# Kernel optimization log

Hardware: AMD Instinct MI355X
Metric: run time of the kernel (lower is better)

## Reference

```python
import jax, jax.numpy as jnp
import numpy as np

N_NODES = 100000
NEG_SLOPE = 0.2

def _glorot(key, shape):
    lim = float(np.sqrt(6.0 / (shape[0] + shape[-1])))
    return jax.random.uniform(key, shape, jnp.float32, -lim, lim)

def setup_inputs() -> dict:
    key = jax.random.key(0)
    ks = jax.random.split(key, 12)
    x = jax.random.normal(ks[0], (N_NODES, 128), jnp.float32)
    edge_index = jax.random.randint(ks[1], (2, 3200000), 0, N_NODES).astype(jnp.int64)
    # layer 1: in=128, heads=2, out=8
    W1 = _glorot(ks[2], (128, 16)); a_src1 = _glorot(ks[3], (2, 8)); a_dst1 = _glorot(ks[4], (2, 8)); b1 = jnp.zeros((16,), jnp.float32)
    # layer 2: in=16, heads=2, out=4
    W2 = _glorot(ks[5], (16, 8)); a_src2 = _glorot(ks[6], (2, 4)); a_dst2 = _glorot(ks[7], (2, 4)); b2 = jnp.zeros((8,), jnp.float32)
    # layer 3: in=8, heads=1, out=4
    W3 = _glorot(ks[8], (8, 4)); a_src3 = _glorot(ks[9], (1, 4)); a_dst3 = _glorot(ks[10], (1, 4)); b3 = jnp.zeros((4,), jnp.float32)
    Wc = _glorot(ks[11], (4, 2)); bc = jnp.zeros((2,), jnp.float32)
    return {"x": x, "edge_index": edge_index,
            "W1": W1, "a_src1": a_src1, "a_dst1": a_dst1, "b1": b1,
            "W2": W2, "a_src2": a_src2, "a_dst2": a_dst2, "b2": b2,
            "W3": W3, "a_src3": a_src3, "a_dst3": a_dst3, "b3": b3,
            "Wc": Wc, "bc": bc}

def gat_layer(x, src, dst, W, a_src, a_dst, b, H, C):
    # PyG GATConv: linear -> per-node attention terms -> per-edge leaky_relu -> segment softmax over dst -> scatter-sum
    N = x.shape[0]
    h = (x @ W).reshape(N, H, C)                         # [N,H,C]
    alpha_s = jnp.sum(h * a_src, axis=-1)                # [N,H]
    alpha_d = jnp.sum(h * a_dst, axis=-1)                # [N,H]
    e = jax.nn.leaky_relu(alpha_s[src] + alpha_d[dst], NEG_SLOPE)  # [E,H]
    m = jax.ops.segment_max(e, dst, num_segments=N)      # [N,H]
    ex = jnp.exp(e - m[dst])
    denom = jax.ops.segment_sum(ex, dst, num_segments=N)
    alpha = ex / (denom[dst] + 1e-16)                    # [E,H]
    out = jax.ops.segment_sum(h[src] * alpha[:, :, None], dst, num_segments=N)  # [N,H,C]
    return out.reshape(N, H * C) + b

def reference(x, edge_index, W1, a_src1, a_dst1, b1, W2, a_src2, a_dst2, b2, W3, a_src3, a_dst3, b3, Wc, bc):
    N = x.shape[0]
    loop = jnp.arange(N, dtype=edge_index.dtype)
    src = jnp.concatenate([edge_index[0], loop])  # add_self_loops=True (PyG default)
    dst = jnp.concatenate([edge_index[1], loop])
    h = jax.nn.relu(gat_layer(x, src, dst, W1, a_src1, a_dst1, b1, 2, 8))
    h = jax.nn.relu(gat_layer(h, src, dst, W2, a_src2, a_dst2, b2, 2, 4))
    # dropout p=0.5 is identity in eval mode
    h = gat_layer(h, src, dst, W3, a_src3, a_dst3, b3, 1, 4)
    return h @ Wc + bc
```

## Files before the change

### kernel.cpp

```cpp
#include <hip/hip_runtime.h>

#define TB 256
#define NGRP 8
#define NB_P 512
#define TBP 256
#define NBKT 256
#define SORT_T 1024
#define STG_CAP 14336
#define STG2_CAP 6400

typedef int      i4v __attribute__((ext_vector_type(4)));
typedef float    f4v __attribute__((ext_vector_type(4)));
typedef _Float16 h4v __attribute__((ext_vector_type(4)));
typedef _Float16 h8v __attribute__((ext_vector_type(8)));

struct __align__(16) Rec2 { _Float16 h[8]; float as[2]; float pad[2]; };
struct __align__(16) Rec3 { _Float16 h[4]; float as; float pad; };

static __device__ __forceinline__ float leaky(float x) {
  return x > 0.f ? x : 0.2f * x;
}


__global__ void k_bcount(const int* __restrict__ dstA, int* __restrict__ cnt,
                         int E4, int E, unsigned M, int CH4) {
  __shared__ int lc[4 * NBKT];
  for (int i = threadIdx.x; i < 4 * NBKT; i += TBP) lc[i] = 0;
  __syncthreads();
  int* lcw = lc + (threadIdx.x >> 6) * NBKT;
  const int bstart = blockIdx.x * CH4;
  const int bend = min(E4, bstart + CH4);
  const i4v* d4 = reinterpret_cast<const i4v*>(dstA);
  for (int i = bstart + threadIdx.x; i < bend; i += TBP) {
    i4v d = __builtin_nontemporal_load(&d4[i]);
#pragma unroll
    for (int k = 0; k < 4; ++k) atomicAdd(&lcw[__umulhi((unsigned)d[k], M)], 1);
  }
  if (blockIdx.x == NB_P - 1) {
    for (int t = E4 * 4 + threadIdx.x; t < E; t += TBP)
      atomicAdd(&lcw[__umulhi((unsigned)dstA[t], M)], 1);
  }
  __syncthreads();
  for (int b = threadIdx.x; b < NBKT; b += TBP)
    cnt[b * NB_P + blockIdx.x] = lc[b] + lc[NBKT + b] + lc[2 * NBKT + b] + lc[3 * NBKT + b];
}

__global__ void k_bscan1(const int* __restrict__ cnt, int* __restrict__ off,
                         int* __restrict__ colTotal) {
  __shared__ int sh[NB_P];
  const int t = threadIdx.x;
  const int b = blockIdx.x;
  int v = cnt[b * NB_P + t];
  sh[t] = v;
  __syncthreads();
  for (int o = 1; o < NB_P; o <<= 1) {
    int u = (t >= o) ? sh[t - o] : 0;
    __syncthreads();
    sh[t] += u;
    __syncthreads();
  }
  off[b * NB_P + t] = sh[t] - v;
  if (t == NB_P - 1) colTotal[b] = sh[t];
}

__global__ void k_bscan2(const int* __restrict__ colTotal, int* __restrict__ bucketBase) {
  __shared__ int sh[NBKT];
  const int t = threadIdx.x;
  int v = colTotal[t];
  sh[t] = v;
  __syncthreads();
  for (int o = 1; o < NBKT; o <<= 1) {
    int u = (t >= o) ? sh[t - o] : 0;
    __syncthreads();
    sh[t] += u;
    __syncthreads();
  }
  bucketBase[t] = sh[t] - v;
  if (t == NBKT - 1) bucketBase[NBKT] = sh[t];
}

__global__ void k_bscatter(const int* __restrict__ srcA, const int* __restrict__ dstA,
                           const int* __restrict__ cnt, const int* __restrict__ off,
                           const int* __restrict__ bucketBase, int* __restrict__ epk,
                           int E4, int E, unsigned M, int R, int CH4) {
  __shared__ int loff[NBKT + 1];
  __shared__ int lcur[NBKT];
  __shared__ int gbase[NBKT];
  __shared__ int stg[STG2_CAP];
  const int t = threadIdx.x;
  {
    int v = cnt[t * NB_P + blockIdx.x];
    loff[t] = v;
    __syncthreads();
    for (int o = 1; o < NBKT; o <<= 1) {
      int u = (t >= o) ? loff[t - o] : 0;
      __syncthreads();
      loff[t] += u;
      __syncthreads();
    }
    int incl = loff[t];
    __syncthreads();
    loff[t] = incl - v;
    lcur[t] = incl - v;
    if (t == NBKT - 1) loff[NBKT] = incl;
    gbase[t] = bucketBase[t] + off[t * NB_P + blockIdx.x];
  }
  __syncthreads();
  const int bstart = blockIdx.x * CH4;
  const int bend = min(E4, bstart + CH4);
  const i4v* d4 = reinterpret_cast<const i4v*>(dstA);
  const i4v* s4 = reinterpret_cast<const i4v*>(srcA);
  for (int i = bstart + t; i < bend; i += TBP) {
    i4v d = __builtin_nontemporal_load(&d4[i]);
    i4v sv = __builtin_nontemporal_load(&s4[i]);
#pragma unroll
    for (int k = 0; k < 4; ++k) {
      int dd = d[k];
      int b = __umulhi((unsigned)dd, M);
      int pos = atomicAdd(&lcur[b], 1);
      stg[pos] = ((dd - b * R) << 17) | sv[k];
    }
  }
  if (blockIdx.x == NB_P - 1) {
    for (int i = E4 * 4 + t; i < E; i += TBP) {
      int dd = dstA[i];
      int b = __umulhi((unsigned)dd, M);
      int pos = atomicAdd(&lcur[b], 1);
      stg[pos] = ((dd - b * R) << 17) | srcA[i];
    }
  }
  __syncthreads();
  const int total = loff[NBKT];
  for (int i = t; i < total; i += TBP) {
    int loQ = 0, hiQ = NBKT;
#pragma unroll
    for (int it = 0; it < 8; ++it) {
      int mid = (loQ + hiQ) >> 1;
      if (loff[mid] <= i) loQ = mid; else hiQ = mid;
    }
    epk[gbase[loQ] + (i - loff[loQ])] = stg[i];
  }
}

__global__ void k_bsort(const int* __restrict__ epk, const int* __restrict__ bucketBase,
                        int* __restrict__ rowStart, int* __restrict__ colIdx,
                        int N, int R, int E) {
  __shared__ int sc[512];
  __shared__ int stg[STG_CAP];
  const int b = (blockIdx.x & (NGRP - 1)) * (NBKT / NGRP) + (blockIdx.x >> 3);
  const int lo = bucketBase[b], hi = bucketBase[b + 1];
  const int cnt = hi - lo;
  const int nodeLo = b * R;
  const int nN = min(R, N - nodeLo);
  const int t = threadIdx.x;
  if (t < 512) sc[t] = 0;
  __syncthreads();
  for (int i = lo + t; i < hi; i += SORT_T) {
    int pk = __builtin_nontemporal_load(&epk[i]);
    atomicAdd(&sc[pk >> 17], 1);
  }
  __syncthreads();
  int own = (t < 512) ? sc[t] : 0;
  for (int o = 1; o < 512; o <<= 1) {
    int u = (t < 512 && t >= o) ? sc[t - o] : 0;
    __syncthreads();
    if (t < 512) sc[t] += u;
    __syncthreads();
  }
  if (t < nN) rowStart[nodeLo + t] = lo + sc[t] - own;
  if (b == NBKT - 1 && t == 0) rowStart[N] = E;
  if (t < 512) sc[t] -= own;
  __syncthreads();
  if (cnt <= STG_CAP) {
    for (int i = lo + t; i < hi; i += SORT_T) {
      int pk = epk[i];
      int pos = atomicAdd(&sc[pk >> 17], 1);
      stg[pos] = pk & 0x1FFFF;
    }
    __syncthreads();
    for (int i = t; i < cnt; i += SORT_T) colIdx[lo + i] = stg[i];
  } else {
    for (int i = lo + t; i < hi; i += SORT_T) {
      int pk = epk[i];
      int pos = lo + atomicAdd(&sc[pk >> 17], 1);
      colIdx[pos] = pk & 0x1FFFF;
    }
  }
}


template <int IN, int H, int C, int SPLIT, bool NT>
__global__ void k_node(const float* __restrict__ xin, const float* __restrict__ W,
                       const float* __restrict__ a_src, const float* __restrict__ a_dst,
                       _Float16* __restrict__ hout, float* __restrict__ as_,
                       float* __restrict__ ad_, int N) {
  constexpr int OUT = H * C;
  constexpr int PIN4 = IN / SPLIT / 4;
  constexpr int NPB = TB / SPLIT;
  __shared__ float Ws[IN * OUT];
  __shared__ float As[OUT], Ad[OUT];
  for (int i = threadIdx.x; i < IN * OUT; i += blockDim.x) Ws[i] = W[i];
  if (threadIdx.x < OUT) {
    As[threadIdx.x] = a_src[threadIdx.x];
    Ad[threadIdx.x] = a_dst[threadIdx.x];
  }
  __syncthreads();
  const int j = threadIdx.x & (SPLIT - 1);
  const int n = blockIdx.x * NPB + threadIdx.x / SPLIT;
  if (n >= N) return;
  float acc[OUT];
#pragma unroll
  for (int q = 0; q < OUT; ++q) acc[q] = 0.f;
  const f4v* x4 = reinterpret_cast<const f4v*>(xin + (size_t)n * IN + j * (IN / SPLIT));
#pragma unroll
  for (int k4 = 0; k4 < PIN4; ++k4) {
    f4v xv = NT ? __builtin_nontemporal_load(&x4[k4]) : x4[k4];
    const int kb = j * (IN / SPLIT) + 4 * k4;
#pragma unroll
    for (int q = 0; q < OUT; ++q) {
      acc[q] += xv[0] * Ws[(kb + 0) * OUT + q];
      acc[q] += xv[1] * Ws[(kb + 1) * OUT + q];
      acc[q] += xv[2] * Ws[(kb + 2) * OUT + q];
      acc[q] += xv[3] * Ws[(kb + 3) * OUT + q];
    }
  }
#pragma unroll
  for (int o = 1; o < SPLIT; o <<= 1) {
#pragma unroll
    for (int q = 0; q < OUT; ++q) acc[q] += __shfl_xor(acc[q], o);
  }
  constexpr int WCH = OUT / 4;
  if (j < WCH) {
    h4v v;
    v[0] = (_Float16)acc[4 * j + 0];
    v[1] = (_Float16)acc[4 * j + 1];
    v[2] = (_Float16)acc[4 * j + 2];
    v[3] = (_Float16)acc[4 * j + 3];
    reinterpret_cast<h4v*>(hout + (size_t)n * OUT)[j] = v;
  }
  if (j < H) {
    float ss = 0.f, dd = 0.f;
#pragma unroll
    for (int c = 0; c < C; ++c) {
      ss += acc[j * C + c] * As[j * C + c];
      dd += acc[j * C + c] * Ad[j * C + c];
    }
    as_[n * H + j] = ss;
    ad_[n * H + j] = dd;
  }
}


__global__ void k_edge12(const int* __restrict__ rowStart, const int* __restrict__ colIdx,
                         const _Float16* __restrict__ h1, const float* __restrict__ as_,
                         const float* __restrict__ ad_, const float* __restrict__ b1,
                         const float* __restrict__ W2, const float* __restrict__ as2w,
                         const float* __restrict__ ad2w, Rec2* __restrict__ r2,
                         float* __restrict__ ad2, int N, int R8) {
  constexpr int L = 2, S = 4, LS = 8, NPB = TB / LS;
  __shared__ float Ws2[128], A2s[8], A2d[8], B1s[16];
  if (threadIdx.x < 128) Ws2[threadIdx.x] = W2[threadIdx.x];
  if (threadIdx.x < 8) {
    A2s[threadIdx.x] = as2w[threadIdx.x];
    A2d[threadIdx.x] = ad2w[threadIdx.x];
  }
  if (threadIdx.x < 16) B1s[threadIdx.x] = b1[threadIdx.x];
  __syncthreads();
  const int g = blockIdx.x & (NGRP - 1);
  const int lb = blockIdx.x / NGRP;
  const int lane = threadIdx.x % LS;
  const int sub = lane >> 1;
  const int j = lane & 1;
  const int n = g * R8 + lb * NPB + threadIdx.x / LS;
  const int nEnd = min((g + 1) * R8, N);
  if (n >= nEnd) return;
  const float adv = ad_[n * 2 + j];
  const int start = rowStart[n];
  const int end = rowStart[n + 1];
  float s = 0.f, acc[8];
#pragma unroll
  for (int q = 0; q < 8; ++q) acc[q] = 0.f;
  if (sub == 0) {
    float p = __expf(leaky(as_[n * 2 + j] + adv));
    h8v a0 = reinterpret_cast<const h8v*>(h1 + (size_t)n * 16)[j];
    s = p;
#pragma unroll
    for (int q = 0; q < 8; ++q) acc[q] = p * (float)a0[q];
  }
  const int base = start & ~3;
  const int nch = (end - base + 3) >> 2;
  for (int t = sub; t < nch; t += S) {
    const int i0 = base + 4 * t;
    i4v cv = *reinterpret_cast<const i4v*>(colIdx + i0);
#pragma unroll
    for (int k = 0; k < 4; ++k) {
      const bool ok = (i0 + k >= start) && (i0 + k < end);
      const int src = ok ? cv[k] : n;
      h8v hv = reinterpret_cast<const h8v*>(h1 + (size_t)src * 16)[j];
      float e = as_[src * 2 + j];
      float p = ok ? __expf(leaky(e + adv)) : 0.f;
      s += p;
#pragma unroll
      for (int q = 0; q < 8; ++q) acc[q] += p * (float)hv[q];
    }
  }
#pragma unroll
  for (int off = L; off < LS; off <<= 1) {
    s += __shfl_xor(s, off);
#pragma unroll
    for (int q = 0; q < 8; ++q) acc[q] += __shfl_xor(acc[q], off);
  }
  if (sub == 0) {
    float inv = 1.f / (s + 1e-16f);
    float o1v[8];
#pragma unroll
    for (int q = 0; q < 8; ++q) o1v[q] = fmaxf(acc[q] * inv + B1s[j * 8 + q], 0.f);
    float h2p[8];
#pragma unroll
    for (int q = 0; q < 8; ++q) {
      float tacc = 0.f;
#pragma unroll
      for (int c = 0; c < 8; ++c) tacc += o1v[c] * Ws2[(j * 8 + c) * 8 + q];
      h2p[q] = tacc;
    }
    float h2f[8];
#pragma unroll
    for (int q = 0; q < 8; ++q) h2f[q] = h2p[q] + __shfl_xor(h2p[q], 1);
    h4v v;
#pragma unroll
    for (int q = 0; q < 4; ++q) v[q] = (_Float16)h2f[j * 4 + q];
    reinterpret_cast<h4v*>(r2[n].h)[j] = v;
    float ss = 0.f, dd = 0.f;
#pragma unroll
    for (int c = 0; c < 4; ++c) {
      ss += h2f[j * 4 + c] * A2s[j * 4 + c];
      dd += h2f[j * 4 + c] * A2d[j * 4 + c];
    }
    r2[n].as[j] = ss;
    ad2[n * 2 + j] = dd;
  }
}


__global__ void k_edge23(const int* __restrict__ rowStart, const int* __restrict__ colIdx,
                         const Rec2* __restrict__ r2, const float* __restrict__ ad_,
                         const float* __restrict__ b2, const float* __restrict__ W3,
                         const float* __restrict__ as3w, const float* __restrict__ ad3w,
                         Rec3* __restrict__ r3, float* __restrict__ ad3, int N, int R8) {
  constexpr int L = 2, S = 4, LS = 8, NPB = TB / LS;
  __shared__ float Ws3[32], A3s[4], A3d[4], B2s[8];
  if (threadIdx.x < 32) Ws3[threadIdx.x] = W3[threadIdx.x];
  if (threadIdx.x < 4) {
    A3s[threadIdx.x] = as3w[threadIdx.x];
    A3d[threadIdx.x] = ad3w[threadIdx.x];
  }
  if (threadIdx.x < 8) B2s[threadIdx.x] = b2[threadIdx.x];
  __syncthreads();
  const int g = blockIdx.x & (NGRP - 1);
  const int lb = blockIdx.x / NGRP;
  const int lane = threadIdx.x % LS;
  const int sub = lane >> 1;
  const int j = lane & 1;
  const int n = g * R8 + lb * NPB + threadIdx.x / LS;
  const int nEnd = min((g + 1) * R8, N);
  if (n >= nEnd) return;
  const float adv = ad_[n * 2 + j];
  const int start = rowStart[n];
  const int end = rowStart[n + 1];
  float s = 0.f, acc[4];
#pragma unroll
  for (int q = 0; q < 4; ++q) acc[q] = 0.f;
  if (sub == 0) {
    float p = __expf(leaky(r2[n].as[j] + adv));
    h4v a0 = reinterpret_cast<const h4v*>(r2[n].h)[j];
    s = p;
#pragma unroll
    for (int q = 0; q < 4; ++q) acc[q] = p * (float)a0[q];
  }
  const int base = start & ~3;
  const int nch = (end - base + 3) >> 2;
  for (int t = sub; t < nch; t += S) {
    const int i0 = base + 4 * t;
    i4v cv = *reinterpret_cast<const i4v*>(colIdx + i0);
#pragma unroll
    for (int k = 0; k < 4; ++k) {
      const bool ok = (i0 + k >= start) && (i0 + k < end);
      const int src = ok ? cv[k] : n;
      h4v hv = reinterpret_cast<const h4v*>(r2[src].h)[j];
      float e = r2[src].as[j];
      float p = ok ? __expf(leaky(e + adv)) : 0.f;
      s += p;
#pragma unroll
      for (int q = 0; q < 4; ++q) acc[q] += p * (float)hv[q];
    }
  }
#pragma unroll
  for (int off = L; off < LS; off <<= 1) {
    s += __shfl_xor(s, off);
#pragma unroll
    for (int q = 0; q < 4; ++q) acc[q] += __shfl_xor(acc[q], off);
  }
  if (sub == 0) {
    float inv = 1.f / (s + 1e-16f);
    float o2v[4];
#pragma unroll
    for (int q = 0; q < 4; ++q) o2v[q] = fmaxf(acc[q] * inv + B2s[j * 4 + q], 0.f);
    float h3p[4];
#pragma unroll
    for (int q = 0; q < 4; ++q) {
      float tacc = 0.f;
#pragma unroll
      for (int c = 0; c < 4; ++c) tacc += o2v[c] * Ws3[(j * 4 + c) * 4 + q];
      h3p[q] = tacc;
    }
    float h3f[4];
#pragma unroll
    for (int q = 0; q < 4; ++q) h3f[q] = h3p[q] + __shfl_xor(h3p[q], 1);
    if (j == 0) {
      Rec3 rec;
#pragma unroll
      for (int q = 0; q < 4; ++q) rec.h[q] = (_Float16)h3f[q];
      float ss = 0.f, dd = 0.f;
#pragma unroll
      for (int c = 0; c < 4; ++c) {
        ss += h3f[c] * A3s[c];
        dd += h3f[c] * A3d[c];
      }
      rec.as = ss;
      rec.pad = 0.f;
      r3[n] = rec;
      ad3[n] = dd;
    }
  }
}


__global__ void k_edge3(const int* __restrict__ rowStart, const int* __restrict__ colIdx,
                        const Rec3* __restrict__ r3, const float* __restrict__ ad_,
                        const float* __restrict__ b3, const float* __restrict__ Wc,
                        const float* __restrict__ bc, float* __restrict__ out,
                        int N, int R8) {
  constexpr int S = 8;
  constexpr int NPB = TB / S;
  const int g = blockIdx.x & (NGRP - 1);
  const int lb = blockIdx.x / NGRP;
  const int sub = threadIdx.x % S;
  const int n = g * R8 + lb * NPB + threadIdx.x / S;
  const int nEnd = min((g + 1) * R8, N);
  if (n >= nEnd) return;
  const float adv = ad_[n];
  const int start = rowStart[n];
  const int end = rowStart[n + 1];
  float s = 0.f, acc0 = 0.f, acc1 = 0.f, acc2 = 0.f, acc3 = 0.f;
  if (sub == 0) {
    Rec3 rec = r3[n];
    float p = __expf(leaky(rec.as + adv));
    s = p;
    acc0 = p * (float)rec.h[0];
    acc1 = p * (float)rec.h[1];
    acc2 = p * (float)rec.h[2];
    acc3 = p * (float)rec.h[3];
  }
  const int base = start & ~3;
  const int nch = (end - base + 3) >> 2;
  for (int t = sub; t < nch; t += S) {
    const int i0 = base + 4 * t;
    i4v cv = *reinterpret_cast<const i4v*>(colIdx + i0);
#pragma unroll
    for (int k = 0; k < 4; ++k) {
      const bool ok = (i0 + k >= start) && (i0 + k < end);
      const int src = ok ? cv[k] : n;
      Rec3 rec = r3[src];
      float p = ok ? __expf(leaky(rec.as + adv)) : 0.f;
      s += p;
      acc0 += p * (float)rec.h[0];
      acc1 += p * (float)rec.h[1];
      acc2 += p * (float)rec.h[2];
      acc3 += p * (float)rec.h[3];
    }
  }
#pragma unroll
  for (int off = 1; off < S; off <<= 1) {
    s += __shfl_xor(s, off);
    acc0 += __shfl_xor(acc0, off);
    acc1 += __shfl_xor(acc1, off);
    acc2 += __shfl_xor(acc2, off);
    acc3 += __shfl_xor(acc3, off);
  }
  if (sub == 0) {
    float inv = 1.f / (s + 1e-16f);
    float o0 = acc0 * inv + b3[0];
    float o1 = acc1 * inv + b3[1];
    float o2 = acc2 * inv + b3[2];
    float o3 = acc3 * inv + b3[3];
    float2 r;
    r.x = o0 * Wc[0] + o1 * Wc[2] + o2 * Wc[4] + o3 * Wc[6] + bc[0];
    r.y = o0 * Wc[1] + o1 * Wc[3] + o2 * Wc[5] + o3 * Wc[7] + bc[1];
    reinterpret_cast<float2*>(out)[n] = r;
  }
}


extern "C" void kernel_launch(void* const* d_in, const int* in_sizes, int n_in,
                              void* d_out, int out_size, void* d_ws, size_t ws_size,
                              hipStream_t stream) {
  const float* x    = (const float*)d_in[0];
  const int*   ei   = (const int*)d_in[1];
  const float* W1   = (const float*)d_in[2];
  const float* as1w = (const float*)d_in[3];
  const float* ad1w = (const float*)d_in[4];
  const float* b1   = (const float*)d_in[5];
  const float* W2   = (const float*)d_in[6];
  const float* as2w = (const float*)d_in[7];
  const float* ad2w = (const float*)d_in[8];
  const float* b2   = (const float*)d_in[9];
  const float* W3   = (const float*)d_in[10];
  const float* as3w = (const float*)d_in[11];
  const float* ad3w = (const float*)d_in[12];
  const float* b3   = (const float*)d_in[13];
  const float* Wc   = (const float*)d_in[14];
  const float* bc   = (const float*)d_in[15];
  float* out = (float*)d_out;

  const int N = in_sizes[0] / 128;
  const int E = in_sizes[1] / 2;
  const int* srcA = ei;
  const int* dstA = ei + E;

  char* p = (char*)d_ws;
  auto alloc = [&](size_t bytes) -> void* {
    void* r = (void*)p;
    p += (bytes + 255) & ~(size_t)255;
    return r;
  };
  int* cnt        = (int*)alloc((size_t)NBKT * NB_P * 4);
  int* off        = (int*)alloc((size_t)NBKT * NB_P * 4);
  int* colTotal   = (int*)alloc(NBKT * 4);
  int* bucketBase = (int*)alloc((NBKT + 1) * 4);
  int* rowStart   = (int*)alloc((size_t)(N + 1) * 4);
  int* epk        = (int*)alloc((size_t)E * 4);
  int* colIdx     = (int*)alloc((size_t)E * 4 + 256);
  _Float16* h1 = (_Float16*)alloc((size_t)N * 16 * 2);
  float* as1 = (float*)alloc((size_t)N * 2 * 4);
  float* ad1 = (float*)alloc((size_t)N * 2 * 4);
  Rec2* r2   = (Rec2*)alloc((size_t)N * sizeof(Rec2));
  float* ad2 = (float*)alloc((size_t)N * 2 * 4);
  Rec3* r3   = (Rec3*)alloc((size_t)N * sizeof(Rec3));
  float* ad3 = (float*)alloc((size_t)N * 4);

  const int R   = (N + NBKT - 1) / NBKT;
  const unsigned M = (unsigned)(((1ULL << 32) + R - 1) / R);
  const int R8  = R * (NBKT / NGRP);
  const int E4  = E >> 2;
  const int CH4 = (E4 + NB_P - 1) / NB_P;

  k_bcount<<<NB_P, TBP, 0, stream>>>(dstA, cnt, E4, E, M, CH4);
  k_bscan1<<<NBKT, NB_P, 0, stream>>>(cnt, off, colTotal);
  k_bscan2<<<1, NBKT, 0, stream>>>(colTotal, bucketBase);
  k_bscatter<<<NB_P, TBP, 0, stream>>>(srcA, dstA, cnt, off, bucketBase, epk, E4, E, M, R, CH4);
  k_bsort<<<NBKT, SORT_T, 0, stream>>>(epk, bucketBase, rowStart, colIdx, N, R, E);

  const int nb1 = (N + (TB / 4) - 1) / (TB / 4);
  const int ge8 = NGRP * ((R8 + (TB / 8) - 1) / (TB / 8));

  k_node<128, 2, 8, 4, true><<<nb1, TB, 0, stream>>>(x, W1, as1w, ad1w, h1, as1, ad1, N);
  k_edge12<<<ge8, TB, 0, stream>>>(rowStart, colIdx, h1, as1, ad1, b1, W2, as2w, ad2w,
                                   r2, ad2, N, R8);
  k_edge23<<<ge8, TB, 0, stream>>>(rowStart, colIdx, r2, ad2, b2, W3, as3w, ad3w,
                                   r3, ad3, N, R8);
  k_edge3<<<ge8, TB, 0, stream>>>(rowStart, colIdx, r3, ad3, b3, Wc, bc, out, N, R8);
}
```

Measured before the change: 177.9 us.

## Merge bucket count with layer-1 node transform and prefetch column indices

Merges the edge bucket-count kernel and the layer-1 node linear transform into one launch, with block ranges split by blockIdx, so the independent dense x@W1 work runs alongside the count pass and one launch is removed. In each of the three edge kernels, the next chunk of column indices is loaded one iteration early to hide index-load latency behind the gathers. The merged kernel shares one shared-memory buffer between the two roles. Prefetching holds an extra vector register per thread.

```diff
diff --git a/kernel.cpp b/kernel.cpp
--- a/kernel.cpp
+++ b/kernel.cpp
@@ -22,27 +22,89 @@
 }
 
 
-__global__ void k_bcount(const int* __restrict__ dstA, int* __restrict__ cnt,
-                         int E4, int E, unsigned M, int CH4) {
-  __shared__ int lc[4 * NBKT];
-  for (int i = threadIdx.x; i < 4 * NBKT; i += TBP) lc[i] = 0;
-  __syncthreads();
-  int* lcw = lc + (threadIdx.x >> 6) * NBKT;
-  const int bstart = blockIdx.x * CH4;
-  const int bend = min(E4, bstart + CH4);
-  const i4v* d4 = reinterpret_cast<const i4v*>(dstA);
-  for (int i = bstart + threadIdx.x; i < bend; i += TBP) {
-    i4v d = __builtin_nontemporal_load(&d4[i]);
-#pragma unroll
-    for (int k = 0; k < 4; ++k) atomicAdd(&lcw[__umulhi((unsigned)d[k], M)], 1);
-  }
-  if (blockIdx.x == NB_P - 1) {
-    for (int t = E4 * 4 + threadIdx.x; t < E; t += TBP)
-      atomicAdd(&lcw[__umulhi((unsigned)dstA[t], M)], 1);
-  }
-  __syncthreads();
-  for (int b = threadIdx.x; b < NBKT; b += TBP)
-    cnt[b * NB_P + blockIdx.x] = lc[b] + lc[NBKT + b] + lc[2 * NBKT + b] + lc[3 * NBKT + b];
+__global__ void __launch_bounds__(TB)
+k_bcount_node1(const int* __restrict__ dstA, int* __restrict__ cnt,
+               int E4, int E, unsigned M, int CH4,
+               const float* __restrict__ xin, const float* __restrict__ W1,
+               const float* __restrict__ a_src, const float* __restrict__ a_dst,
+               _Float16* __restrict__ hout, float* __restrict__ as_,
+               float* __restrict__ ad_, int N) {
+  __shared__ __align__(16) char smem[8448];
+  if (blockIdx.x < NB_P) {
+    int* lc = (int*)smem;
+    for (int i = threadIdx.x; i < 4 * NBKT; i += TBP) lc[i] = 0;
+    __syncthreads();
+    int* lcw = lc + (threadIdx.x >> 6) * NBKT;
+    const int bstart = blockIdx.x * CH4;
+    const int bend = min(E4, bstart + CH4);
+    const i4v* d4 = reinterpret_cast<const i4v*>(dstA);
+    for (int i = bstart + threadIdx.x; i < bend; i += TBP) {
+      i4v d = __builtin_nontemporal_load(&d4[i]);
+#pragma unroll
+      for (int k = 0; k < 4; ++k) atomicAdd(&lcw[__umulhi((unsigned)d[k], M)], 1);
+    }
+    if (blockIdx.x == NB_P - 1) {
+      for (int t = E4 * 4 + threadIdx.x; t < E; t += TBP)
+        atomicAdd(&lcw[__umulhi((unsigned)dstA[t], M)], 1);
+    }
+    __syncthreads();
+    for (int b = threadIdx.x; b < NBKT; b += TBP)
+      cnt[b * NB_P + blockIdx.x] = lc[b] + lc[NBKT + b] + lc[2 * NBKT + b] + lc[3 * NBKT + b];
+  } else {
+    constexpr int IN = 128, OUT = 16, SPLIT = 4, NPB = TB / SPLIT, PIN4 = IN / SPLIT / 4;
+    float* Ws = (float*)smem;
+    float* As = (float*)(smem + 8192);
+    float* Ad = (float*)(smem + 8256);
+    const int bid = blockIdx.x - NB_P;
+    for (int i = threadIdx.x; i < IN * OUT; i += TB) Ws[i] = W1[i];
+    if (threadIdx.x < OUT) {
+      As[threadIdx.x] = a_src[threadIdx.x];
+      Ad[threadIdx.x] = a_dst[threadIdx.x];
+    }
+    __syncthreads();
+    const int j = threadIdx.x & (SPLIT - 1);
+    const int n = bid * NPB + threadIdx.x / SPLIT;
+    if (n >= N) return;
+    float acc[OUT];
+#pragma unroll
+    for (int q = 0; q < OUT; ++q) acc[q] = 0.f;
+    const f4v* x4 = reinterpret_cast<const f4v*>(xin + (size_t)n * IN + j * (IN / SPLIT));
+#pragma unroll
+    for (int k4 = 0; k4 < PIN4; ++k4) {
+      f4v xv = __builtin_nontemporal_load(&x4[k4]);
+      const int kb = j * (IN / SPLIT) + 4 * k4;
+#pragma unroll
+      for (int q = 0; q < OUT; ++q) {
+        acc[q] += xv[0] * Ws[(kb + 0) * OUT + q];
+        acc[q] += xv[1] * Ws[(kb + 1) * OUT + q];
+        acc[q] += xv[2] * Ws[(kb + 2) * OUT + q];
+        acc[q] += xv[3] * Ws[(kb + 3) * OUT + q];
+      }
+    }
+#pragma unroll
+    for (int o = 1; o < SPLIT; o <<= 1) {
+#pragma unroll
+      for (int q = 0; q < OUT; ++q) acc[q] += __shfl_xor(acc[q], o);
+    }
+    if (j < OUT / 4) {
+      h4v v;
+      v[0] = (_Float16)acc[4 * j + 0];
+      v[1] = (_Float16)acc[4 * j + 1];
+      v[2] = (_Float16)acc[4 * j + 2];
+      v[3] = (_Float16)acc[4 * j + 3];
+      reinterpret_cast<h4v*>(hout + (size_t)n * OUT)[j] = v;
+    }
+    if (j < 2) {
+      float ss = 0.f, dd = 0.f;
+#pragma unroll
+      for (int c = 0; c < 8; ++c) {
+        ss += acc[j * 8 + c] * As[j * 8 + c];
+        dd += acc[j * 8 + c] * Ad[j * 8 + c];
+      }
+      as_[n * 2 + j] = ss;
+      ad_[n * 2 + j] = dd;
+    }
+  }
 }
 
 __global__ void k_bscan1(const int* __restrict__ cnt, int* __restrict__ off,
@@ -189,68 +251,6 @@
 }
 
 
-template <int IN, int H, int C, int SPLIT, bool NT>
-__global__ void k_node(const float* __restrict__ xin, const float* __restrict__ W,
-                       const float* __restrict__ a_src, const float* __restrict__ a_dst,
-                       _Float16* __restrict__ hout, float* __restrict__ as_,
-                       float* __restrict__ ad_, int N) {
-  constexpr int OUT = H * C;
-  constexpr int PIN4 = IN / SPLIT / 4;
-  constexpr int NPB = TB / SPLIT;
-  __shared__ float Ws[IN * OUT];
-  __shared__ float As[OUT], Ad[OUT];
-  for (int i = threadIdx.x; i < IN * OUT; i += blockDim.x) Ws[i] = W[i];
-  if (threadIdx.x < OUT) {
-    As[threadIdx.x] = a_src[threadIdx.x];
-    Ad[threadIdx.x] = a_dst[threadIdx.x];
-  }
-  __syncthreads();
-  const int j = threadIdx.x & (SPLIT - 1);
-  const int n = blockIdx.x * NPB + threadIdx.x / SPLIT;
-  if (n >= N) return;
-  float acc[OUT];
-#pragma unroll
-  for (int q = 0; q < OUT; ++q) acc[q] = 0.f;
-  const f4v* x4 = reinterpret_cast<const f4v*>(xin + (size_t)n * IN + j * (IN / SPLIT));
-#pragma unroll
-  for (int k4 = 0; k4 < PIN4; ++k4) {
-    f4v xv = NT ? __builtin_nontemporal_load(&x4[k4]) : x4[k4];
-    const int kb = j * (IN / SPLIT) + 4 * k4;
-#pragma unroll
-    for (int q = 0; q < OUT; ++q) {
-      acc[q] += xv[0] * Ws[(kb + 0) * OUT + q];
-      acc[q] += xv[1] * Ws[(kb + 1) * OUT + q];
-      acc[q] += xv[2] * Ws[(kb + 2) * OUT + q];
-      acc[q] += xv[3] * Ws[(kb + 3) * OUT + q];
-    }
-  }
-#pragma unroll
-  for (int o = 1; o < SPLIT; o <<= 1) {
-#pragma unroll
-    for (int q = 0; q < OUT; ++q) acc[q] += __shfl_xor(acc[q], o);
-  }
-  constexpr int WCH = OUT / 4;
-  if (j < WCH) {
-    h4v v;
-    v[0] = (_Float16)acc[4 * j + 0];
-    v[1] = (_Float16)acc[4 * j + 1];
-    v[2] = (_Float16)acc[4 * j + 2];
-    v[3] = (_Float16)acc[4 * j + 3];
-    reinterpret_cast<h4v*>(hout + (size_t)n * OUT)[j] = v;
-  }
-  if (j < H) {
-    float ss = 0.f, dd = 0.f;
-#pragma unroll
-    for (int c = 0; c < C; ++c) {
-      ss += acc[j * C + c] * As[j * C + c];
-      dd += acc[j * C + c] * Ad[j * C + c];
-    }
-    as_[n * H + j] = ss;
-    ad_[n * H + j] = dd;
-  }
-}
-
-
 __global__ void k_edge12(const int* __restrict__ rowStart, const int* __restrict__ colIdx,
                          const _Float16* __restrict__ h1, const float* __restrict__ as_,
                          const float* __restrict__ ad_, const float* __restrict__ b1,
@@ -289,9 +289,12 @@
   }
   const int base = start & ~3;
   const int nch = (end - base + 3) >> 2;
+  i4v cv;
+  if (sub < nch) cv = *reinterpret_cast<const i4v*>(colIdx + base + 4 * sub);
   for (int t = sub; t < nch; t += S) {
+    i4v nxt = cv;
+    if (t + S < nch) nxt = *reinterpret_cast<const i4v*>(colIdx + base + 4 * (t + S));
     const int i0 = base + 4 * t;
-    i4v cv = *reinterpret_cast<const i4v*>(colIdx + i0);
 #pragma unroll
     for (int k = 0; k < 4; ++k) {
       const bool ok = (i0 + k >= start) && (i0 + k < end);
@@ -303,6 +306,7 @@
 #pragma unroll
       for (int q = 0; q < 8; ++q) acc[q] += p * (float)hv[q];
     }
+    cv = nxt;
   }
 #pragma unroll
   for (int off = L; off < LS; off <<= 1) {
@@ -379,9 +383,12 @@
   }
   const int base = start & ~3;
   const int nch = (end - base + 3) >> 2;
+  i4v cv;
+  if (sub < nch) cv = *reinterpret_cast<const i4v*>(colIdx + base + 4 * sub);
   for (int t = sub; t < nch; t += S) {
+    i4v nxt = cv;
+    if (t + S < nch) nxt = *reinterpret_cast<const i4v*>(colIdx + base + 4 * (t + S));
     const int i0 = base + 4 * t;
-    i4v cv = *reinterpret_cast<const i4v*>(colIdx + i0);
 #pragma unroll
     for (int k = 0; k < 4; ++k) {
       const bool ok = (i0 + k >= start) && (i0 + k < end);
@@ -393,6 +400,7 @@
 #pragma unroll
       for (int q = 0; q < 4; ++q) acc[q] += p * (float)hv[q];
     }
+    cv = nxt;
   }
 #pragma unroll
   for (int off = L; off < LS; off <<= 1) {
@@ -463,9 +471,12 @@
   }
   const int base = start & ~3;
   const int nch = (end - base + 3) >> 2;
+  i4v cv;
+  if (sub < nch) cv = *reinterpret_cast<const i4v*>(colIdx + base + 4 * sub);
   for (int t = sub; t < nch; t += S) {
+    i4v nxt = cv;
+    if (t + S < nch) nxt = *reinterpret_cast<const i4v*>(colIdx + base + 4 * (t + S));
     const int i0 = base + 4 * t;
-    i4v cv = *reinterpret_cast<const i4v*>(colIdx + i0);
 #pragma unroll
     for (int k = 0; k < 4; ++k) {
       const bool ok = (i0 + k >= start) && (i0 + k < end);
@@ -478,6 +489,7 @@
       acc2 += p * (float)rec.h[2];
       acc3 += p * (float)rec.h[3];
     }
+    cv = nxt;
   }
 #pragma unroll
   for (int off = 1; off < S; off <<= 1) {
@@ -554,16 +566,16 @@
   const int E4  = E >> 2;
   const int CH4 = (E4 + NB_P - 1) / NB_P;
 
-  k_bcount<<<NB_P, TBP, 0, stream>>>(dstA, cnt, E4, E, M, CH4);
+  const int nb1 = (N + (TB / 4) - 1) / (TB / 4);
+  const int ge8 = NGRP * ((R8 + (TB / 8) - 1) / (TB / 8));
+
+  k_bcount_node1<<<NB_P + nb1, TB, 0, stream>>>(dstA, cnt, E4, E, M, CH4,
+                                                x, W1, as1w, ad1w, h1, as1, ad1, N);
   k_bscan1<<<NBKT, NB_P, 0, stream>>>(cnt, off, colTotal);
   k_bscan2<<<1, NBKT, 0, stream>>>(colTotal, bucketBase);
   k_bscatter<<<NB_P, TBP, 0, stream>>>(srcA, dstA, cnt, off, bucketBase, epk, E4, E, M, R, CH4);
   k_bsort<<<NBKT, SORT_T, 0, stream>>>(epk, bucketBase, rowStart, colIdx, N, R, E);
 
-  const int nb1 = (N + (TB / 4) - 1) / (TB / 4);
-  const int ge8 = NGRP * ((R8 + (TB / 8) - 1) / (TB / 8));
-
-  k_node<128, 2, 8, 4, true><<<nb1, TB, 0, stream>>>(x, W1, as1w, ad1w, h1, as1, ad1, N);
   k_edge12<<<ge8, TB, 0, stream>>>(rowStart, colIdx, h1, as1, ad1, b1, W2, as2w, ad2w,
                                    r2, ad2, N, R8);
   k_edge23<<<ge8, TB, 0, stream>>>(rowStart, colIdx, r2, ad2, b2, W3, as3w, ad3w,
```

New measurement: 172.2 us. -3.2%, faster.
